# Kernel tuning notes

Hardware: AMD Instinct MI355X
Metric: run time of the kernel (lower is better)

Reference implementation:

```python
import jax, jax.numpy as jnp
import numpy as np

B, DIN, DOUT, E, H, K = 8192, 1024, 1024, 8, 128, 2

def setup_inputs() -> dict:
    key = jax.random.key(0)
    ks = jax.random.split(key, 6)
    s = 0.02
    return {
        "x": jax.random.normal(ks[0], (B, DIN), jnp.float32),
        "w1": jax.random.normal(ks[1], (DIN, H), jnp.float32) * s,
        "b1": jnp.zeros((H,), jnp.float32),
        "wg": jax.random.normal(ks[2], (DIN, H), jnp.float32) * s,
        "bg": jnp.zeros((H,), jnp.float32),
        "w2": jax.random.normal(ks[3], (H, E), jnp.float32) * s,
        "b2": jnp.zeros((E,), jnp.float32),
        "we": jax.random.normal(ks[4], (E, DIN, DOUT), jnp.float32) * s,
        "be": jnp.zeros((E, DOUT), jnp.float32),
    }

def reference(x, w1, b1, wg, bg, w2, b2, we, be):
    Bx = x.shape[0]
    Eo = we.shape[0]
    Do = we.shape[2]
    # Router with GLU; NOTE: softmax over BATCH dim (dim=0), as in source.
    h = (x @ w1 + b1) * jax.nn.relu(x @ wg + bg)
    h = jax.nn.relu(h)
    l = jax.nn.softmax(x=(h @ w2 + b2), axis=0)  # [B, E]
    batch_K = -(-K * Bx) // Eo  # ceil(K/E * B), static
    # top-k tokens per expert (along batch dim)
    ws_t, ib_t = jax.lax.top_k(l.T, batch_K)  # [E, bK]
    ws, ib = ws_t.T, ib_t.T                   # [bK, E]
    nws = jax.nn.softmax(ws, axis=0)          # renorm over selected tokens
    # dispatch: gather selected tokens for all experts at once
    sel = x[ib]                                # [bK, E, DIN]
    eo = jnp.einsum('ked,edo->keo', sel, we) + be  # [bK, E, DOUT]
    eo = eo * nws[:, :, None]
    # combine (concat_sum): per-expert scatter-set + shared scatter-add sum
    e_idx = jnp.broadcast_to(jnp.arange(Eo)[None, :], ib.shape)  # [bK, E]
    out_e = jnp.zeros((Eo, Bx, Do), x.dtype).at[e_idx, ib].set(eo)
    temp_sum = jnp.zeros((Bx, Do), x.dtype).at[ib].add(eo)
    out_e = out_e + temp_sum[None]
    return out_e.transpose(1, 0, 2).reshape(Bx, Eo * Do)
```

## Files before the change

### kernel.cpp

```cpp
#include <hip/hip_runtime.h>
#include <math.h>

#define B_TOK 8192
#define D_IN 1024
#define D_OUT 1024
#define N_E 8
#define N_H 128
#define SEL 2048

using bf16x8 = __attribute__((ext_vector_type(8))) short;
using floatx4 = __attribute__((ext_vector_type(4))) float;

__device__ __forceinline__ unsigned short f2bf(float f) {
  unsigned u = __float_as_uint(f);
  u = (u + 0x7FFFu + ((u >> 16) & 1u)) >> 16;
  return (unsigned short)u;
}

__device__ __forceinline__ float bf2f(unsigned short h) {
  return __uint_as_float(((unsigned)h) << 16);
}

__device__ __forceinline__ void async_cp16(const void* g, void* l) {
  __builtin_amdgcn_global_load_lds((__attribute__((address_space(1))) void*)g,
                                   (__attribute__((address_space(3))) void*)l,
                                   16, 0, 0);
}

__global__ __launch_bounds__(256) void k_cast_weT(const float* __restrict__ we,
                                                  unsigned short* __restrict__ web) {
  __shared__ float tile[64][68];
  const int e = blockIdx.z;
  const float* wsrc = we + (size_t)e * D_IN * D_OUT;
  unsigned short* wdst = web + (size_t)e * D_OUT * D_IN;
  const int t = threadIdx.x;
  const int r = t >> 4;
  const int c = (t & 15) * 4;
  const int d0 = blockIdx.x * 64, o0 = blockIdx.y * 64;
#pragma unroll
  for (int p = 0; p < 4; ++p) {
    float4 v = *(const float4*)(wsrc + (size_t)(d0 + r + 16 * p) * D_OUT + o0 + c);
    tile[r + 16 * p][c] = v.x; tile[r + 16 * p][c + 1] = v.y;
    tile[r + 16 * p][c + 2] = v.z; tile[r + 16 * p][c + 3] = v.w;
  }
  __syncthreads();
#pragma unroll
  for (int p = 0; p < 4; ++p) {
    int orow = r + 16 * p;
    ushort4 v;
    v.x = f2bf(tile[c + 0][orow]); v.y = f2bf(tile[c + 1][orow]);
    v.z = f2bf(tile[c + 2][orow]); v.w = f2bf(tile[c + 3][orow]);
    *(ushort4*)(wdst + (size_t)(o0 + orow) * D_IN + d0 + c) = v;
  }
}

__global__ __launch_bounds__(256) void k_router(const float* __restrict__ x,
                                                const float* __restrict__ w1,
                                                const float* __restrict__ b1,
                                                const float* __restrict__ wg,
                                                const float* __restrict__ bg,
                                                const float* __restrict__ w2,
                                                const float* __restrict__ b2,
                                                unsigned short* __restrict__ xb,
                                                double* __restrict__ logits) {
  __shared__ float xs[16][36];
  __shared__ float ws1[32][128];
  __shared__ float wsg[32][128];
  __shared__ float w2s[N_H * N_E];
  const int t = threadIdx.x;
  const int b0 = blockIdx.x * 16;
  const int tg = t >> 5;
  const int og = t & 31;

  ((float4*)w2s)[t] = ((const float4*)w2)[t];

  double d1[2][4] = {}; double dg[2][4] = {};
  for (int k0 = 0; k0 < D_IN; k0 += 32) {
    __syncthreads();
    if (t < 128) {
      int r = t >> 3, c = (t & 7) * 4;
      float4 v = *(const float4*)(x + (size_t)(b0 + r) * D_IN + k0 + c);
      *(float4*)(&xs[r][c]) = v;
      ushort4 u; u.x = f2bf(v.x); u.y = f2bf(v.y); u.z = f2bf(v.z); u.w = f2bf(v.w);
      *(ushort4*)(xb + (size_t)(b0 + r) * D_IN + k0 + c) = u;
    }
    {
      int r = t >> 5, c = (t & 31) * 4;
#pragma unroll
      for (int p = 0; p < 4; ++p) {
        *(float4*)(&ws1[r + 8 * p][c]) = *(const float4*)(w1 + (size_t)(k0 + r + 8 * p) * N_H + c);
        *(float4*)(&wsg[r + 8 * p][c]) = *(const float4*)(wg + (size_t)(k0 + r + 8 * p) * N_H + c);
      }
    }
    __syncthreads();
    float a1[2][4] = {}; float ag[2][4] = {};
    for (int k = 0; k < 32; k += 4) {
      float xk[2][4];
#pragma unroll
      for (int i = 0; i < 2; ++i) {
        float4 v = *(const float4*)(&xs[tg * 2 + i][k]);
        xk[i][0] = v.x; xk[i][1] = v.y; xk[i][2] = v.z; xk[i][3] = v.w;
      }
#pragma unroll
      for (int kk = 0; kk < 4; ++kk) {
        float4 w1v = *(const float4*)(&ws1[k + kk][og * 4]);
        float4 wgv = *(const float4*)(&wsg[k + kk][og * 4]);
        float wa1[4] = {w1v.x, w1v.y, w1v.z, w1v.w};
        float wag[4] = {wgv.x, wgv.y, wgv.z, wgv.w};
#pragma unroll
        for (int i = 0; i < 2; ++i) {
#pragma unroll
          for (int j = 0; j < 4; ++j) {
            a1[i][j] += xk[i][kk] * wa1[j];
            ag[i][j] += xk[i][kk] * wag[j];
          }
        }
      }
    }
#pragma unroll
    for (int i = 0; i < 2; ++i)
#pragma unroll
      for (int j = 0; j < 4; ++j) { d1[i][j] += a1[i][j]; dg[i][j] += ag[i][j]; }
  }

  float4 b1v = *(const float4*)(b1 + og * 4);
  float4 bgv = *(const float4*)(bg + og * 4);
  float b1a[4] = {b1v.x, b1v.y, b1v.z, b1v.w};
  float bga[4] = {bgv.x, bgv.y, bgv.z, bgv.w};
  float hv[2][4];
#pragma unroll
  for (int i = 0; i < 2; ++i) {
#pragma unroll
    for (int j = 0; j < 4; ++j) {
      float a = (float)d1[i][j] + b1a[j];
      float g = (float)dg[i][j] + bga[j];
      g = fmaxf(g, 0.f);
      hv[i][j] = fmaxf(a * g, 0.f);
    }
  }

  double lp[2][8] = {};
#pragma unroll
  for (int i = 0; i < 2; ++i) {
#pragma unroll
    for (int j = 0; j < 4; ++j) {
      double hj = (double)hv[i][j];
      int kk = og * 4 + j;
#pragma unroll
      for (int e = 0; e < 8; ++e)
        lp[i][e] += hj * (double)w2s[kk * N_E + e];
    }
  }
#pragma unroll
  for (int o = 16; o; o >>= 1) {
#pragma unroll
    for (int i = 0; i < 2; ++i)
#pragma unroll
      for (int e = 0; e < 8; ++e)
        lp[i][e] += __shfl_down(lp[i][e], o);
  }
  if (og == 0) {
#pragma unroll
    for (int i = 0; i < 2; ++i)
#pragma unroll
      for (int e = 0; e < 8; ++e)
        logits[(size_t)(b0 + tg * 2 + i) * N_E + e] = lp[i][e] + (double)b2[e];
  }
}

__global__ __launch_bounds__(256) void k_topk(const double* __restrict__ logits,
                                              int* __restrict__ ib, float* __restrict__ nws,
                                              int* __restrict__ slot) {
  const int e = blockIdx.x;
  const int t = threadIdx.x;
  __shared__ double redd[4];
  __shared__ int redi[4];
  __shared__ unsigned redu[4];
  __shared__ int s_cnt;

  double lv[32];
#pragma unroll
  for (int i = 0; i < 32; ++i) lv[i] = logits[(size_t)(t + i * 256) * N_E + e];

  double m = -1e300;
#pragma unroll
  for (int i = 0; i < 32; ++i) m = fmax(m, lv[i]);
  for (int o = 32; o; o >>= 1) m = fmax(m, __shfl_down(m, o));
  __syncthreads();
  if ((t & 63) == 0) redd[t >> 6] = m;
  __syncthreads();
  const double maxl = fmax(fmax(redd[0], redd[1]), fmax(redd[2], redd[3]));

  double s = 0.0;
#pragma unroll
  for (int i = 0; i < 32; ++i) s += exp(lv[i] - maxl);
  for (int o = 32; o; o >>= 1) s += __shfl_down(s, o);
  __syncthreads();
  if ((t & 63) == 0) redd[t >> 6] = s;
  __syncthreads();
  const double sum = redd[0] + redd[1] + redd[2] + redd[3];

  unsigned kr[32];
#pragma unroll
  for (int i = 0; i < 32; ++i) {
    float lf = (float)(exp(lv[i] - maxl) / sum);
    kr[i] = __float_as_uint(lf);
  }

  unsigned thr = 0;
  for (int bit = 31; bit >= 0; --bit) {
    unsigned trial = thr | (1u << bit);
    int c = 0;
#pragma unroll
    for (int i = 0; i < 32; ++i) c += (kr[i] >= trial) ? 1 : 0;
    for (int o = 32; o; o >>= 1) c += __shfl_down(c, o);
    __syncthreads();
    if ((t & 63) == 0) redi[t >> 6] = c;
    __syncthreads();
    c = redi[0] + redi[1] + redi[2] + redi[3];
    if (c >= SEL) thr = trial;
  }

  int c1 = 0;
#pragma unroll
  for (int i = 0; i < 32; ++i) c1 += (kr[i] > thr) ? 1 : 0;
  for (int o = 32; o; o >>= 1) c1 += __shfl_down(c1, o);
  __syncthreads();
  if ((t & 63) == 0) redi[t >> 6] = c1;
  __syncthreads();
  c1 = redi[0] + redi[1] + redi[2] + redi[3];
  const int need = SEL - c1;

  int cut = 0;
  for (int bit = 12; bit >= 0; --bit) {
    int trial = cut | (1 << bit);
    int c = 0;
#pragma unroll
    for (int i = 0; i < 32; ++i) c += (kr[i] == thr && (t + i * 256) < trial) ? 1 : 0;
    for (int o = 32; o; o >>= 1) c += __shfl_down(c, o);
    __syncthreads();
    if ((t & 63) == 0) redi[t >> 6] = c;
    __syncthreads();
    c = redi[0] + redi[1] + redi[2] + redi[3];
    if (c < need) cut = trial;
  }

  unsigned mk = 0;
#pragma unroll
  for (int i = 0; i < 32; ++i) mk = (kr[i] > mk) ? kr[i] : mk;
  for (int o = 32; o; o >>= 1) { unsigned v = __shfl_down(mk, o); mk = (v > mk) ? v : mk; }
  __syncthreads();
  if ((t & 63) == 0) redu[t >> 6] = mk;
  __syncthreads();
  mk = redu[0]; if (redu[1] > mk) mk = redu[1]; if (redu[2] > mk) mk = redu[2]; if (redu[3] > mk) mk = redu[3];
  const double maxw = (double)__uint_as_float(mk);

  double ss = 0.0;
#pragma unroll
  for (int i = 0; i < 32; ++i) {
    int idx = t + i * 256;
    bool sel = (kr[i] > thr) || (kr[i] == thr && idx <= cut);
    if (sel) ss += exp((double)__uint_as_float(kr[i]) - maxw);
  }
  for (int o = 32; o; o >>= 1) ss += __shfl_down(ss, o);
  __syncthreads();
  if ((t & 63) == 0) redd[t >> 6] = ss;
  __syncthreads();
  const double ssum = redd[0] + redd[1] + redd[2] + redd[3];

  if (t == 0) s_cnt = 0;
#pragma unroll
  for (int i = 0; i < 32; ++i) slot[(size_t)(t + i * 256) * N_E + e] = -1;
  __syncthreads();
  for (int i = 0; i < 32; ++i) {
    int idx = t + i * 256;
    bool sel = (kr[i] > thr) || (kr[i] == thr && idx <= cut);
    if (sel) {
      int pos = atomicAdd(&s_cnt, 1);
      ib[e * SEL + pos] = idx;
      nws[e * SEL + pos] = (float)(exp((double)__uint_as_float(kr[i]) - maxw) / ssum);
      slot[(size_t)idx * N_E + e] = pos;
    }
  }
}

__global__ __launch_bounds__(256) void k_expert_gemm(const unsigned short* __restrict__ xb,
                                                     const unsigned short* __restrict__ web,
                                                     const float* __restrict__ be,
                                                     const int* __restrict__ ib,
                                                     const float* __restrict__ nws,
                                                     unsigned short* __restrict__ eo) {
  __shared__ unsigned short As[128 * 64];
  __shared__ unsigned short Bs[128 * 64];
  __shared__ int rowidx[128];
  __shared__ float nwss[128];
  const int e = blockIdx.z;
  const int bm = blockIdx.x * 128;
  const int bn = blockIdx.y * 128;
  const int t = threadIdx.x;
  const int wave = t >> 6, lane = t & 63;
  if (t < 128) {
    rowidx[t] = ib[e * SEL + bm + t];
    nwss[t] = nws[e * SEL + bm + t];
  }
  __syncthreads();
  const unsigned short* wbase = web + (size_t)e * D_IN * D_OUT;
  const int chunk = lane & 7;
  const unsigned short* aptr[4];
  const unsigned short* bptr[4];
  unsigned short* adst[4];
  unsigned short* bdst[4];
#pragma unroll
  for (int c = 0; c < 4; ++c) {
    int row = c * 32 + wave * 8 + (lane >> 3);
    aptr[c] = xb + (size_t)rowidx[row] * D_IN + chunk * 8;
    bptr[c] = wbase + (size_t)(bn + row) * D_IN + chunk * 8;
    adst[c] = As + row * 64 + chunk * 8;
    bdst[c] = Bs + row * 64 + chunk * 8;
  }
  floatx4 acc[4][4] = {};
  const int wm = wave >> 1, wn = wave & 1;
  const int fr = lane & 15, fq = lane >> 4;

  for (int k0 = 0; k0 < D_IN; k0 += 64) {
#pragma unroll
    for (int c = 0; c < 4; ++c) {
      async_cp16(aptr[c] + k0, adst[c]);
      async_cp16(bptr[c] + k0, bdst[c]);
    }
    __syncthreads();
#pragma unroll
    for (int kk = 0; kk < 2; ++kk) {
      bf16x8 af[4], bfr[4];
#pragma unroll
      for (int mt = 0; mt < 4; ++mt)
        af[mt] = *(const bf16x8*)(As + (wm * 64 + mt * 16 + fr) * 64 + kk * 32 + fq * 8);
#pragma unroll
      for (int nt = 0; nt < 4; ++nt)
        bfr[nt] = *(const bf16x8*)(Bs + (wn * 64 + nt * 16 + fr) * 64 + kk * 32 + fq * 8);
#pragma unroll
      for (int mt = 0; mt < 4; ++mt)
#pragma unroll
        for (int nt = 0; nt < 4; ++nt)
          acc[mt][nt] = __builtin_amdgcn_mfma_f32_16x16x32_bf16(af[mt], bfr[nt], acc[mt][nt], 0, 0, 0);
    }
    __syncthreads();
  }
  float bev[4];
#pragma unroll
  for (int nt = 0; nt < 4; ++nt) bev[nt] = be[e * D_OUT + bn + wn * 64 + nt * 16 + fr];
#pragma unroll
  for (int mt = 0; mt < 4; ++mt) {
#pragma unroll
    for (int r = 0; r < 4; ++r) {
      int lrow = wm * 64 + mt * 16 + fq * 4 + r;
      float nw = nwss[lrow];
      size_t rbase = ((size_t)e * SEL + bm + lrow) * D_OUT;
#pragma unroll
      for (int nt = 0; nt < 4; ++nt) {
        int cc = bn + wn * 64 + nt * 16 + fr;
        eo[rbase + cc] = f2bf((acc[mt][nt][r] + bev[nt]) * nw);
      }
    }
  }
}

__global__ __launch_bounds__(256) void k_combine(const unsigned short* __restrict__ eo,
                                                 const int* __restrict__ slot,
                                                 float* __restrict__ out) {
  const int b = blockIdx.x;
  const int t = threadIdx.x;
  __shared__ int ss[8];
  if (t < 8) ss[t] = slot[(size_t)b * N_E + t];
  __syncthreads();
  const int d0 = t * 4;
  float vx[8], vy[8], vz[8], vw[8];
  float tx = 0.f, ty = 0.f, tz = 0.f, tw = 0.f;
#pragma unroll
  for (int e = 0; e < 8; ++e) {
    int k = ss[e];
    if (k >= 0) {
      ushort4 u = *(const ushort4*)(eo + ((size_t)e * SEL + k) * D_OUT + d0);
      vx[e] = bf2f(u.x); vy[e] = bf2f(u.y); vz[e] = bf2f(u.z); vw[e] = bf2f(u.w);
      tx += vx[e]; ty += vy[e]; tz += vz[e]; tw += vw[e];
    } else {
      vx[e] = 0.f; vy[e] = 0.f; vz[e] = 0.f; vw[e] = 0.f;
    }
  }
#pragma unroll
  for (int e = 0; e < 8; ++e) {
    float4 o;
    o.x = tx + vx[e]; o.y = ty + vy[e]; o.z = tz + vz[e]; o.w = tw + vw[e];
    *(float4*)(out + (size_t)b * (N_E * D_OUT) + e * D_OUT + d0) = o;
  }
}

extern "C" void kernel_launch(void* const* d_in, const int* in_sizes, int n_in,
                              void* d_out, int out_size, void* d_ws, size_t ws_size,
                              hipStream_t stream) {
  const float* x  = (const float*)d_in[0];
  const float* w1 = (const float*)d_in[1];
  const float* b1 = (const float*)d_in[2];
  const float* wg = (const float*)d_in[3];
  const float* bg = (const float*)d_in[4];
  const float* w2 = (const float*)d_in[5];
  const float* b2 = (const float*)d_in[6];
  const float* we = (const float*)d_in[7];
  const float* be = (const float*)d_in[8];
  float* out = (float*)d_out;

  char* ws = (char*)d_ws;
  size_t off = 0;
  auto alloc = [&](size_t bytes) -> void* {
    void* p = ws + off;
    off += (bytes + 255) & ~(size_t)255;
    return p;
  };
  unsigned short* xb  = (unsigned short*)alloc((size_t)B_TOK * D_IN * 2);
  unsigned short* web = (unsigned short*)alloc((size_t)N_E * D_IN * D_OUT * 2);
  unsigned short* eo  = (unsigned short*)alloc((size_t)N_E * SEL * D_OUT * 2);
  double* lgts  = (double*)alloc((size_t)B_TOK * N_E * 8);
  int* ibuf     = (int*)alloc((size_t)N_E * SEL * 4);
  float* nws    = (float*)alloc((size_t)N_E * SEL * 4);
  int* slot     = (int*)alloc((size_t)B_TOK * N_E * 4);
  if (off > ws_size) return;

  hipLaunchKernelGGL(k_cast_weT, dim3(16, 16, N_E), dim3(256), 0, stream, we, web);
  hipLaunchKernelGGL(k_router, dim3(B_TOK / 16), dim3(256), 0, stream,
                     x, w1, b1, wg, bg, w2, b2, xb, lgts);
  hipLaunchKernelGGL(k_topk, dim3(N_E), dim3(256), 0, stream, lgts, ibuf, nws, slot);
  hipLaunchKernelGGL(k_expert_gemm, dim3(SEL / 128, D_OUT / 128, N_E), dim3(256), 0, stream,
                     xb, web, be, ibuf, nws, eo);
  hipLaunchKernelGGL(k_combine, dim3(B_TOK), dim3(256), 0, stream, eo, slot, out);
}
```

Before: 535.2 us.

## Fuse expert-weight cast into router kernel and shorten top-k radix search

Merges the expert weight transpose/bf16-cast kernel into the router kernel as extra blocks, so the two independent jobs share one launch and can run concurrently. In the top-k kernel, the bit-by-bit threshold search now starts from the highest bit where the min and max keys differ, which skips the leading iterations. The tie-break index search is skipped when every key equal to the threshold is needed. The max key is reused from the new min/max reduction. The trade-off is a larger shared-memory footprint for all fused blocks, which may lower router occupancy.

```diff
diff --git a/kernel.cpp b/kernel.cpp
--- a/kernel.cpp
+++ b/kernel.cpp
@@ -27,47 +27,53 @@
                                    16, 0, 0);
 }
 
-__global__ __launch_bounds__(256) void k_cast_weT(const float* __restrict__ we,
-                                                  unsigned short* __restrict__ web) {
-  __shared__ float tile[64][68];
-  const int e = blockIdx.z;
-  const float* wsrc = we + (size_t)e * D_IN * D_OUT;
-  unsigned short* wdst = web + (size_t)e * D_OUT * D_IN;
+__global__ __launch_bounds__(256) void k_router_fat(const float* __restrict__ x,
+                                                    const float* __restrict__ w1,
+                                                    const float* __restrict__ b1,
+                                                    const float* __restrict__ wg,
+                                                    const float* __restrict__ bg,
+                                                    const float* __restrict__ w2,
+                                                    const float* __restrict__ b2,
+                                                    const float* __restrict__ we,
+                                                    unsigned short* __restrict__ xb,
+                                                    double* __restrict__ logits,
+                                                    unsigned short* __restrict__ web) {
+  __shared__ char smem[39168];
   const int t = threadIdx.x;
-  const int r = t >> 4;
-  const int c = (t & 15) * 4;
-  const int d0 = blockIdx.x * 64, o0 = blockIdx.y * 64;
-#pragma unroll
-  for (int p = 0; p < 4; ++p) {
-    float4 v = *(const float4*)(wsrc + (size_t)(d0 + r + 16 * p) * D_OUT + o0 + c);
-    tile[r + 16 * p][c] = v.x; tile[r + 16 * p][c + 1] = v.y;
-    tile[r + 16 * p][c + 2] = v.z; tile[r + 16 * p][c + 3] = v.w;
-  }
-  __syncthreads();
-#pragma unroll
-  for (int p = 0; p < 4; ++p) {
-    int orow = r + 16 * p;
-    ushort4 v;
-    v.x = f2bf(tile[c + 0][orow]); v.y = f2bf(tile[c + 1][orow]);
-    v.z = f2bf(tile[c + 2][orow]); v.w = f2bf(tile[c + 3][orow]);
-    *(ushort4*)(wdst + (size_t)(o0 + orow) * D_IN + d0 + c) = v;
-  }
-}
-
-__global__ __launch_bounds__(256) void k_router(const float* __restrict__ x,
-                                                const float* __restrict__ w1,
-                                                const float* __restrict__ b1,
-                                                const float* __restrict__ wg,
-                                                const float* __restrict__ bg,
-                                                const float* __restrict__ w2,
-                                                const float* __restrict__ b2,
-                                                unsigned short* __restrict__ xb,
-                                                double* __restrict__ logits) {
-  __shared__ float xs[16][36];
-  __shared__ float ws1[32][128];
-  __shared__ float wsg[32][128];
-  __shared__ float w2s[N_H * N_E];
-  const int t = threadIdx.x;
+
+  if (blockIdx.x >= 512) {
+    const int wb = blockIdx.x - 512;
+    const int e = wb >> 8;
+    const int rem = wb & 255;
+    const int o0 = (rem >> 4) * 64;
+    const int d0 = (rem & 15) * 64;
+    float (*tile)[68] = (float(*)[68])smem;
+    const float* wsrc = we + (size_t)e * D_IN * D_OUT;
+    unsigned short* wdst = web + (size_t)e * D_OUT * D_IN;
+    const int r = t >> 4;
+    const int c = (t & 15) * 4;
+#pragma unroll
+    for (int p = 0; p < 4; ++p) {
+      float4 v = *(const float4*)(wsrc + (size_t)(d0 + r + 16 * p) * D_OUT + o0 + c);
+      tile[r + 16 * p][c] = v.x; tile[r + 16 * p][c + 1] = v.y;
+      tile[r + 16 * p][c + 2] = v.z; tile[r + 16 * p][c + 3] = v.w;
+    }
+    __syncthreads();
+#pragma unroll
+    for (int p = 0; p < 4; ++p) {
+      int orow = r + 16 * p;
+      ushort4 v;
+      v.x = f2bf(tile[c + 0][orow]); v.y = f2bf(tile[c + 1][orow]);
+      v.z = f2bf(tile[c + 2][orow]); v.w = f2bf(tile[c + 3][orow]);
+      *(ushort4*)(wdst + (size_t)(o0 + orow) * D_IN + d0 + c) = v;
+    }
+    return;
+  }
+
+  float (*xs)[36]  = (float(*)[36])(smem);
+  float (*ws1)[128] = (float(*)[128])(smem + 2304);
+  float (*wsg)[128] = (float(*)[128])(smem + 2304 + 16384);
+  float* w2s = (float*)(smem + 2304 + 16384 + 16384);
   const int b0 = blockIdx.x * 16;
   const int tg = t >> 5;
   const int og = t & 31;
@@ -207,8 +213,33 @@
     kr[i] = __float_as_uint(lf);
   }
 
-  unsigned thr = 0;
-  for (int bit = 31; bit >= 0; --bit) {
+  unsigned mnk = 0xFFFFFFFFu, mxk = 0;
+#pragma unroll
+  for (int i = 0; i < 32; ++i) { mnk = (kr[i] < mnk) ? kr[i] : mnk; mxk = (kr[i] > mxk) ? kr[i] : mxk; }
+  for (int o = 32; o; o >>= 1) {
+    unsigned v = __shfl_down(mnk, o); mnk = (v < mnk) ? v : mnk;
+    unsigned w = __shfl_down(mxk, o); mxk = (w > mxk) ? w : mxk;
+  }
+  __syncthreads();
+  if ((t & 63) == 0) redu[t >> 6] = mnk;
+  __syncthreads();
+  mnk = redu[0]; if (redu[1] < mnk) mnk = redu[1]; if (redu[2] < mnk) mnk = redu[2]; if (redu[3] < mnk) mnk = redu[3];
+  __syncthreads();
+  if ((t & 63) == 0) redu[t >> 6] = mxk;
+  __syncthreads();
+  mxk = redu[0]; if (redu[1] > mxk) mxk = redu[1]; if (redu[2] > mxk) mxk = redu[2]; if (redu[3] > mxk) mxk = redu[3];
+
+  const unsigned diff = mnk ^ mxk;
+  int hb = -1;
+  unsigned thr;
+  if (diff == 0) {
+    thr = mnk;
+  } else {
+    hb = 31 - __clz(diff);
+    thr = mxk & ~((hb >= 31) ? 0xFFFFFFFFu : ((1u << (hb + 1)) - 1u));
+  }
+
+  for (int bit = hb; bit >= 0; --bit) {
     unsigned trial = thr | (1u << bit);
     int c = 0;
 #pragma unroll
@@ -221,39 +252,40 @@
     if (c >= SEL) thr = trial;
   }
 
-  int c1 = 0;
-#pragma unroll
-  for (int i = 0; i < 32; ++i) c1 += (kr[i] > thr) ? 1 : 0;
-  for (int o = 32; o; o >>= 1) c1 += __shfl_down(c1, o);
-  __syncthreads();
-  if ((t & 63) == 0) redi[t >> 6] = c1;
+  int c1 = 0, ceq = 0;
+#pragma unroll
+  for (int i = 0; i < 32; ++i) {
+    c1 += (kr[i] > thr) ? 1 : 0;
+    ceq += (kr[i] == thr) ? 1 : 0;
+  }
+  for (int o = 32; o; o >>= 1) { c1 += __shfl_down(c1, o); ceq += __shfl_down(ceq, o); }
+  __syncthreads();
+  if ((t & 63) == 0) { redi[t >> 6] = c1; ((int*)redu)[t >> 6] = ceq; }
   __syncthreads();
   c1 = redi[0] + redi[1] + redi[2] + redi[3];
+  ceq = ((int*)redu)[0] + ((int*)redu)[1] + ((int*)redu)[2] + ((int*)redu)[3];
   const int need = SEL - c1;
 
-  int cut = 0;
-  for (int bit = 12; bit >= 0; --bit) {
-    int trial = cut | (1 << bit);
-    int c = 0;
-#pragma unroll
-    for (int i = 0; i < 32; ++i) c += (kr[i] == thr && (t + i * 256) < trial) ? 1 : 0;
-    for (int o = 32; o; o >>= 1) c += __shfl_down(c, o);
-    __syncthreads();
-    if ((t & 63) == 0) redi[t >> 6] = c;
-    __syncthreads();
-    c = redi[0] + redi[1] + redi[2] + redi[3];
-    if (c < need) cut = trial;
-  }
-
-  unsigned mk = 0;
-#pragma unroll
-  for (int i = 0; i < 32; ++i) mk = (kr[i] > mk) ? kr[i] : mk;
-  for (int o = 32; o; o >>= 1) { unsigned v = __shfl_down(mk, o); mk = (v > mk) ? v : mk; }
-  __syncthreads();
-  if ((t & 63) == 0) redu[t >> 6] = mk;
-  __syncthreads();
-  mk = redu[0]; if (redu[1] > mk) mk = redu[1]; if (redu[2] > mk) mk = redu[2]; if (redu[3] > mk) mk = redu[3];
-  const double maxw = (double)__uint_as_float(mk);
+  int cut;
+  if (ceq == need) {
+    cut = B_TOK;
+  } else {
+    cut = 0;
+    for (int bit = 12; bit >= 0; --bit) {
+      int trial = cut | (1 << bit);
+      int c = 0;
+#pragma unroll
+      for (int i = 0; i < 32; ++i) c += (kr[i] == thr && (t + i * 256) < trial) ? 1 : 0;
+      for (int o = 32; o; o >>= 1) c += __shfl_down(c, o);
+      __syncthreads();
+      if ((t & 63) == 0) redi[t >> 6] = c;
+      __syncthreads();
+      c = redi[0] + redi[1] + redi[2] + redi[3];
+      if (c < need) cut = trial;
+    }
+  }
+
+  const double maxw = (double)__uint_as_float(mxk);
 
   double ss = 0.0;
 #pragma unroll
@@ -425,9 +457,8 @@
   int* slot     = (int*)alloc((size_t)B_TOK * N_E * 4);
   if (off > ws_size) return;
 
-  hipLaunchKernelGGL(k_cast_weT, dim3(16, 16, N_E), dim3(256), 0, stream, we, web);
-  hipLaunchKernelGGL(k_router, dim3(B_TOK / 16), dim3(256), 0, stream,
-                     x, w1, b1, wg, bg, w2, b2, xb, lgts);
+  hipLaunchKernelGGL(k_router_fat, dim3(512 + 2048), dim3(256), 0, stream,
+                     x, w1, b1, wg, bg, w2, b2, we, xb, lgts, web);
   hipLaunchKernelGGL(k_topk, dim3(N_E), dim3(256), 0, stream, lgts, ibuf, nws, slot);
   hipLaunchKernelGGL(k_expert_gemm, dim3(SEL / 128, D_OUT / 128, N_E), dim3(256), 0, stream,
                      xb, web, be, ibuf, nws, eo);
```

Result: faster. 516.3 us (-3.5%).
